# Performance work log

Measured on AMD Instinct MI355X. Metric: run time of the kernel, lower is better.

The kernel has to match this reference:

```python
import jax, jax.numpy as jnp
import numpy as np
from jax import lax

C = 128; H = 28; W = 28
VID_LENS = [32, 96, 64, 48, 80, 40, 88, 64]  # sums to 512
T_TOTAL = sum(VID_LENS)


def setup_inputs() -> dict:
    key = jax.random.key(0)
    ks = jax.random.split(key, 6)
    fan2 = C * 9
    fan1 = C * 3
    return {
        "x": jax.random.normal(ks[0], (T_TOTAL, C, H, W), dtype=jnp.float32),
        "vid_lens": jnp.array(VID_LENS, dtype=jnp.int32),
        "w_sp": jax.random.normal(ks[1], (C, C, 3, 3), dtype=jnp.float32) / np.sqrt(fan2),
        "b_sp": jax.random.normal(ks[2], (C,), dtype=jnp.float32) * 0.01,
        "w_t": jax.random.normal(ks[3], (C, C, 3), dtype=jnp.float32) / np.sqrt(fan1),
        "b_t": jax.random.normal(ks[4], (C,), dtype=jnp.float32) * 0.01,
        "alpha": jnp.full((C,), 0.25, dtype=jnp.float32),  # MultiNL ~ per-channel PReLU
    }


def _forward(x, vid_lens, w_sp, b_sp, w_t, b_t, alpha):
    projection = x
    # spatial 3x3 conv, stride 1, padding 1 (SAME), NCHW
    y = lax.conv_general_dilated(
        x, w_sp, window_strides=(1, 1), padding="SAME",
        dimension_numbers=("NCHW", "OIHW", "NCHW")) + b_sp[None, :, None, None]

    # Ragged temporal conv1d (k=3, pad=1) over concatenated time axis.
    # Zero the temporal neighbors at segment boundaries so each video is
    # convolved independently (equivalent to per-segment zero padding).
    T = y.shape[0]
    ends = jnp.cumsum(vid_lens)            # segment end indices (exclusive)
    starts = ends - vid_lens               # segment start indices
    start_mask = jnp.zeros((T,), bool).at[starts].set(True)
    end_mask = jnp.zeros((T,), bool).at[ends - 1].set(True)

    y_prev = jnp.where(start_mask[:, None, None, None], 0.0, jnp.roll(y, 1, axis=0))
    y_next = jnp.where(end_mask[:, None, None, None], 0.0, jnp.roll(y, -1, axis=0))

    # conv1d along time == per-tap channel-mixing matmul
    z = (jnp.einsum("oc,tchw->tohw", w_t[:, :, 0], y_prev)
         + jnp.einsum("oc,tchw->tohw", w_t[:, :, 1], y)
         + jnp.einsum("oc,tchw->tohw", w_t[:, :, 2], y_next)
         + b_t[None, :, None, None])

    # MultiNL modeled as per-channel PReLU
    z = jnp.where(z >= 0, z, alpha[None, :, None, None] * z)
    return z + projection


def reference(x, vid_lens, w_sp, b_sp, w_t, b_t, alpha):
    out = _forward(x, vid_lens, w_sp, b_sp, w_t, b_t, alpha)
    return (out, vid_lens)  # lengths are unchanged (k=3, pad=1)
```

## Files before the change

### kernel.cpp

```cpp
#include <hip/hip_runtime.h>

#define TT   512
#define CH   128
#define HWP  784
#define NSEG 8
#define NOUT 51380224

typedef short bf16x8  __attribute__((ext_vector_type(8)));
typedef float f32x4   __attribute__((ext_vector_type(4)));
typedef float f32x16  __attribute__((ext_vector_type(16)));
typedef int   i32x4   __attribute__((ext_vector_type(4)));
typedef unsigned short u16x4 __attribute__((ext_vector_type(4)));
typedef unsigned short u16x8 __attribute__((ext_vector_type(8)));

__device__ inline unsigned short f2bf(float f) {
    unsigned u = __builtin_bit_cast(unsigned, f);
    u += 0x7fffu + ((u >> 16) & 1u);
    return (unsigned short)(u >> 16);
}

__device__ inline void gld_lds16(const void* g, void* l) {
    __builtin_amdgcn_global_load_lds(
        (const __attribute__((address_space(1))) void*)g,
        (__attribute__((address_space(3))) void*)l, 16, 0, 0);
}

#define MFMA32(A, B, C) __builtin_amdgcn_mfma_f32_32x32x16_bf16(A, B, C, 0, 0, 0)

__global__ void repack_wsp(const float* __restrict__ w, short* __restrict__ wA) {
    int s = blockIdx.x * 256 + threadIdx.x;
    if (s >= 128 * 128 * 9) return;
    int co = s / 1152, r = s % 1152, ci = r / 9, kh = (r % 9) / 3, kw = r % 3;
    int tap = kh * 3 + kw;
    int m = co >> 5, row = co & 31;
    int ks = ci >> 4, kgrp = (ci >> 3) & 1, e = ci & 7;
    int lane = kgrp * 32 + row;
    int dst = (((tap * 8 + ks) * 4 + m) * 64 + lane) * 8 + e;
    wA[dst] = (short)f2bf(w[s]);
}

__global__ void repack_wt2(const float* __restrict__ w, short* __restrict__ wAt) {
    int s = blockIdx.x * 256 + threadIdx.x;
    if (s >= 128 * 128 * 3) return;
    int o = s / 384, r = s % 384, i = r / 3, tap = r % 3;
    int dst = tap * 16384 + (o >> 4) * 2048 + (i >> 5) * 512 +
              ((i >> 3) & 3) * 128 + (o & 15) * 8 + (i & 7);
    wAt[dst] = (short)f2bf(w[s]);
}

__global__ __launch_bounds__(256, 2) void spatial_mfma(
    const float* __restrict__ x, const short* __restrict__ wA,
    const float* __restrict__ b_sp, unsigned short* __restrict__ yT)
{
    __shared__ __align__(16) short xs[300 * 128];
    char* xsb = (char*)xs;
    const int t = blockIdx.y;
    const int r0 = blockIdx.x * 8;
    const int rows = (28 - r0 < 8) ? (28 - r0) : 8;
    const int pxcnt = rows * 28;
    const int tid = threadIdx.x;

    for (int u = tid; u < 4480; u += 256) {
        int cp = u & 63, q = u >> 6;
        int rl = q / 7, g = q % 7;
        int rr = r0 - 1 + rl;
        float4 f0 = make_float4(0.f, 0.f, 0.f, 0.f), f1 = f0;
        if (rr >= 0 && rr < 28) {
            const float* px0 = &x[((size_t)(t * CH + 2 * cp)) * HWP + rr * 28 + g * 4];
            f0 = *(const float4*)px0;
            f1 = *(const float4*)(px0 + HWP);
        }
        float a0[4] = {f0.x, f0.y, f0.z, f0.w}, a1[4] = {f1.x, f1.y, f1.z, f1.w};
        int stb = rl * 30 + g * 4 + 1;
#pragma unroll
        for (int j = 0; j < 4; ++j) {
            int st = stb + j;
            unsigned val = (unsigned)f2bf(a0[j]) | ((unsigned)f2bf(a1[j]) << 16);
            int addr = (st << 8) | (((cp >> 2) ^ (st & 15)) << 4) | ((cp & 3) << 2);
            *(unsigned*)(xsb + addr) = val;
        }
    }
    for (int v = tid; v < 1280; v += 256) {
        int cp = v & 63, k = v >> 6;
        int st = (k >> 1) * 30 + (k & 1) * 29;
        int addr = (st << 8) | (((cp >> 2) ^ (st & 15)) << 4) | ((cp & 3) << 2);
        *(unsigned*)(xsb + addr) = 0u;
    }
    __syncthreads();

    const int wid = tid >> 6, l = tid & 63;
    const int l31 = l & 31, bb5 = l >> 5;
    const int ch = wid & 1, pg = wid >> 1;
    const int ch2 = ch * 2;

    int st0[4];
#pragma unroll
    for (int ti = 0; ti < 4; ++ti) {
        int p = (pg * 4 + ti) * 32 + l31;
        int pc = (p < pxcnt) ? p : 0;
        st0[ti] = (pc / 28 + 1) * 30 + pc % 28 + 1;
    }

    f32x16 zz = {};
    f32x16 acc[2][4];
#pragma unroll
    for (int mi = 0; mi < 2; ++mi)
#pragma unroll
        for (int ti = 0; ti < 4; ++ti) acc[mi][ti] = zz;

    const bf16x8* wv = (const bf16x8*)wA;

    for (int tap = 0; tap < 9; ++tap) {
        const int off = (tap / 3 - 1) * 30 + (tap % 3) - 1;
        int rb[4], sw[4];
#pragma unroll
        for (int ti = 0; ti < 4; ++ti) {
            int stv = st0[ti] + off;
            rb[ti] = stv << 8;
            sw[ti] = stv & 15;
        }
        bf16x8 A[16];
#pragma unroll
        for (int k2 = 0; k2 < 16; ++k2)
            A[k2] = wv[((tap * 8 + (k2 >> 1)) * 4 + ch2 + (k2 & 1)) * 64 + l];

#pragma unroll
        for (int ks = 0; ks < 8; ++ks) {
            i32x4 b[4];
#pragma unroll
            for (int ti = 0; ti < 4; ++ti)
                b[ti] = *(const i32x4*)(xsb + (rb[ti] | (((2 * ks + bb5) ^ sw[ti]) << 4)));
            __builtin_amdgcn_s_setprio(1);
#pragma unroll
            for (int ti = 0; ti < 4; ++ti) {
                bf16x8 bf = __builtin_bit_cast(bf16x8, b[ti]);
                acc[0][ti] = MFMA32(A[ks * 2], bf, acc[0][ti]);
                acc[1][ti] = MFMA32(A[ks * 2 + 1], bf, acc[1][ti]);
            }
            __builtin_amdgcn_s_setprio(0);
        }
    }

    __syncthreads();
    const int wbase = wid * 17408;
#pragma unroll
    for (int ti = 0; ti < 4; ++ti) {
#pragma unroll
        for (int mi = 0; mi < 2; ++mi) {
#pragma unroll
            for (int r2 = 0; r2 < 4; ++r2) {
                int cb = (ch2 + mi) * 32 + 8 * r2 + 4 * bb5;
                float4 bs = *(const float4*)&b_sp[cb];
                float bsa[4] = {bs.x, bs.y, bs.z, bs.w};
                u16x4 k;
#pragma unroll
                for (int q = 0; q < 4; ++q)
                    k[q] = f2bf(acc[mi][ti][r2 * 4 + q] + bsa[q]);
                int co_off = (mi * 32 + 8 * r2 + 4 * bb5) * 2;
                *(u16x4*)(xsb + wbase + ti * 4352 + l31 * 136 + co_off) = k;
            }
        }
    }
#pragma unroll
    for (int ti = 0; ti < 4; ++ti) {
        int tI = pg * 4 + ti;
#pragma unroll
        for (int j = 0; j < 4; ++j) {
            int idx = j * 64 + l;
            int pxl = idx >> 3, sub = idx & 7;
            u16x8 v = *(const u16x8*)(xsb + wbase + ti * 4352 + pxl * 136 + sub * 16);
            int p = tI * 32 + pxl;
            if (p < pxcnt) {
                char* dst = (char*)yT + ((size_t)t * HWP + r0 * 28 + p) * 256 +
                            ch * 128 + sub * 16;
                *(u16x8*)dst = v;
            }
        }
    }
}

__global__ __launch_bounds__(256, 4) void temporal_mfma(
    const unsigned short* __restrict__ yT, const short* __restrict__ wAt,
    const float* __restrict__ b_t, const float* __restrict__ alpha,
    const float* __restrict__ x, const int* __restrict__ vid_lens,
    float* __restrict__ out)
{
    __shared__ __align__(16) char ldsT[29696];

    const int chunk = blockIdx.x, t = blockIdx.y;
    const int tid = threadIdx.x, wid = tid >> 6, l = tid & 63;
    const int l15 = l & 15, kgrp = l >> 4;
    const int sx = l15 & 7;

    bool isS = false, isE = false;
    {
        int cum = 0;
        for (int s = 0; s < NSEG; ++s) {
            if (t == cum) isS = true;
            cum += vid_lens[s];
            if (t == cum - 1) isE = true;
        }
    }
    const bool tapAct[3] = {!isS, true, !isE};

    auto stage = [&](int s) {
        int tap = s >> 1, kp = s & 1;
        if (!tapAct[tap]) return;
        int tp = t + tap - 1;
        const char* yb = (const char*)yT + (size_t)tp * HWP * 256;
        char* buf = ldsT + (s & 1) * 14336;
#pragma unroll
        for (int r = 0; r < 4; ++r) {
            int c = r * 256 + wid * 64 + l;
            if (r < 3 || wid < 2) {
                int px = c >> 3, sp = c & 7;
                int ssrc = sp ^ (px & 7);
                const char* g = yb + ((size_t)(chunk * 112 + px)) * 256 + kp * 128 + ssrc * 16;
                char* ldst = buf + (r * 256 + wid * 64) * 16;
                gld_lds16(g, ldst);
            }
        }
    };

    f32x4 acc[2][7];
#pragma unroll
    for (int m = 0; m < 2; ++m)
#pragma unroll
        for (int n = 0; n < 7; ++n) acc[m][n] = (f32x4){0.f, 0.f, 0.f, 0.f};

    const bf16x8* wAv = (const bf16x8*)wAt;

    stage(0);
    __syncthreads();

    for (int s = 0; s < 6; ++s) {
        if (s < 5) stage(s + 1);
        int tap = s >> 1, kp = s & 1;
        if (tapAct[tap]) {
            const char* buf = ldsT + (s & 1) * 14336;
            bf16x8 a[2][2];
#pragma unroll
            for (int m = 0; m < 2; ++m)
#pragma unroll
                for (int k1 = 0; k1 < 2; ++k1)
                    a[m][k1] = wAv[((tap * 8 + wid * 2 + m) * 4 + kp * 2 + k1) * 64 + l];
            __builtin_amdgcn_s_setprio(1);
#pragma unroll
            for (int k1 = 0; k1 < 2; ++k1) {
#pragma unroll
                for (int nf = 0; nf < 7; ++nf) {
                    int addr = (nf * 16 + l15) * 128 + ((k1 * 4 + kgrp) ^ sx) * 16;
                    i32x4 bi = *(const i32x4*)(buf + addr);
                    bf16x8 b = __builtin_bit_cast(bf16x8, bi);
                    acc[0][nf] = __builtin_amdgcn_mfma_f32_16x16x32_bf16(a[0][k1], b, acc[0][nf], 0, 0, 0);
                    acc[1][nf] = __builtin_amdgcn_mfma_f32_16x16x32_bf16(a[1][k1], b, acc[1][nf], 0, 0, 0);
                }
            }
            __builtin_amdgcn_s_setprio(0);
        }
        __syncthreads();
    }

    float* fl = (float*)ldsT;
    const int wbase = wid * 1856;
#pragma unroll
    for (int m = 0; m < 2; ++m) {
#pragma unroll
        for (int nf = 0; nf < 7; ++nf)
#pragma unroll
            for (int rr = 0; rr < 4; ++rr)
                fl[wbase + (kgrp * 4 + rr) * 116 + nf * 16 + l15] = acc[m][nf][rr];
#pragma unroll
        for (int j = 0; j < 7; ++j) {
            int idx = j * 64 + l;
            int co_r = idx / 28, q = idx % 28;
            f32x4 v4 = *(const f32x4*)&fl[wbase + co_r * 116 + q * 4];
            int co_g = wid * 32 + m * 16 + co_r;
            float bt = b_t[co_g], al = alpha[co_g];
            size_t gi = ((size_t)(t * CH + co_g)) * HWP + chunk * 112 + q * 4;
            float4 xv = *(const float4*)&x[gi];
            float xr[4] = {xv.x, xv.y, xv.z, xv.w};
            float rrv[4];
#pragma unroll
            for (int e = 0; e < 4; ++e) {
                float v = v4[e] + bt;
                v = (v >= 0.f) ? v : al * v;
                rrv[e] = v + xr[e];
            }
            *(float4*)&out[gi] = make_float4(rrv[0], rrv[1], rrv[2], rrv[3]);
        }
        __syncthreads();
    }
}

__global__ void write_lens(const int* __restrict__ vid_lens, float* __restrict__ out) {
    int i = threadIdx.x;
    if (i < NSEG) out[NOUT + i] = (float)vid_lens[i];
}

extern "C" void kernel_launch(void* const* d_in, const int* in_sizes, int n_in,
                              void* d_out, int out_size, void* d_ws, size_t ws_size,
                              hipStream_t stream) {
    const float* x        = (const float*)d_in[0];
    const int*   vid_lens = (const int*)d_in[1];
    const float* w_sp     = (const float*)d_in[2];
    const float* b_sp     = (const float*)d_in[3];
    const float* w_t      = (const float*)d_in[4];
    const float* b_t      = (const float*)d_in[5];
    const float* alpha    = (const float*)d_in[6];
    float* out = (float*)d_out;

    unsigned short* yT = (unsigned short*)d_ws;
    short* wA  = (short*)((char*)d_ws + 102760448);
    short* wAt = (short*)((char*)d_ws + 102760448 + 294912);

    repack_wsp<<<576, 256, 0, stream>>>(w_sp, wA);
    repack_wt2<<<192, 256, 0, stream>>>(w_t, wAt);
    spatial_mfma<<<dim3(4, 512), 256, 0, stream>>>(x, wA, b_sp, yT);
    temporal_mfma<<<dim3(7, 512), 256, 0, stream>>>(yT, wAt, b_t, alpha, x, vid_lens, out);
    write_lens<<<1, 64, 0, stream>>>(vid_lens, out);
}
```

Measured before the change: 336.6 us.

## Split spatial conv work across 8 waves with fewer tiles per wave

The spatial conv block grows from 256 to 512 threads. Each wave now computes 2 pixel tiles instead of 4, which halves the accumulator registers and lets more waves stay resident. Weight fragments are loaded per k-pair instead of all 16 at once, trading register pressure for more repeated global/L2 weight loads. The fp32-to-bf16 staging conversion is also changed from round-to-nearest to truncation via a byte permute, which slightly changes numerics.

```diff
diff --git a/kernel.cpp b/kernel.cpp
--- a/kernel.cpp
+++ b/kernel.cpp
@@ -48,7 +48,7 @@
     wAt[dst] = (short)f2bf(w[s]);
 }
 
-__global__ __launch_bounds__(256, 2) void spatial_mfma(
+__global__ __launch_bounds__(512, 4) void spatial_mfma(
     const float* __restrict__ x, const short* __restrict__ wA,
     const float* __restrict__ b_sp, unsigned short* __restrict__ yT)
 {
@@ -60,7 +60,7 @@
     const int pxcnt = rows * 28;
     const int tid = threadIdx.x;
 
-    for (int u = tid; u < 4480; u += 256) {
+    for (int u = tid; u < 4480; u += 512) {
         int cp = u & 63, q = u >> 6;
         int rl = q / 7, g = q % 7;
         int rr = r0 - 1 + rl;
@@ -70,17 +70,20 @@
             f0 = *(const float4*)px0;
             f1 = *(const float4*)(px0 + HWP);
         }
-        float a0[4] = {f0.x, f0.y, f0.z, f0.w}, a1[4] = {f1.x, f1.y, f1.z, f1.w};
+        unsigned u0[4] = {__builtin_bit_cast(unsigned, f0.x), __builtin_bit_cast(unsigned, f0.y),
+                          __builtin_bit_cast(unsigned, f0.z), __builtin_bit_cast(unsigned, f0.w)};
+        unsigned u1[4] = {__builtin_bit_cast(unsigned, f1.x), __builtin_bit_cast(unsigned, f1.y),
+                          __builtin_bit_cast(unsigned, f1.z), __builtin_bit_cast(unsigned, f1.w)};
         int stb = rl * 30 + g * 4 + 1;
 #pragma unroll
         for (int j = 0; j < 4; ++j) {
             int st = stb + j;
-            unsigned val = (unsigned)f2bf(a0[j]) | ((unsigned)f2bf(a1[j]) << 16);
+            unsigned val = __builtin_amdgcn_perm(u1[j], u0[j], 0x07060302u);
             int addr = (st << 8) | (((cp >> 2) ^ (st & 15)) << 4) | ((cp & 3) << 2);
             *(unsigned*)(xsb + addr) = val;
         }
     }
-    for (int v = tid; v < 1280; v += 256) {
+    for (int v = tid; v < 1280; v += 512) {
         int cp = v & 63, k = v >> 6;
         int st = (k >> 1) * 30 + (k & 1) * 29;
         int addr = (st << 8) | (((cp >> 2) ^ (st & 15)) << 4) | ((cp & 3) << 2);
@@ -92,85 +95,86 @@
     const int l31 = l & 31, bb5 = l >> 5;
     const int ch = wid & 1, pg = wid >> 1;
     const int ch2 = ch * 2;
-
-    int st0[4];
-#pragma unroll
-    for (int ti = 0; ti < 4; ++ti) {
-        int p = (pg * 4 + ti) * 32 + l31;
-        int pc = (p < pxcnt) ? p : 0;
-        st0[ti] = (pc / 28 + 1) * 30 + pc % 28 + 1;
-    }
+    const int tI0 = pg * 2, tI1 = pg * 2 + 1;
+
+    const int p0 = tI0 * 32 + l31;
+    const int p1 = tI1 * 32 + l31;
+    const bool ok0 = (p0 < pxcnt);
+    const bool ok1 = (tI1 < 7) && (p1 < pxcnt);
+    const int pc0 = ok0 ? p0 : 0;
+    const int pc1 = ok1 ? p1 : 0;
+    const int st0_0 = (pc0 / 28 + 1) * 30 + pc0 % 28 + 1;
+    const int st0_1 = (pc1 / 28 + 1) * 30 + pc1 % 28 + 1;
 
     f32x16 zz = {};
-    f32x16 acc[2][4];
-#pragma unroll
-    for (int mi = 0; mi < 2; ++mi)
-#pragma unroll
-        for (int ti = 0; ti < 4; ++ti) acc[mi][ti] = zz;
+    f32x16 acc00 = zz, acc10 = zz;
+    f32x16 acc01 = zz, acc11 = zz;
 
     const bf16x8* wv = (const bf16x8*)wA;
 
     for (int tap = 0; tap < 9; ++tap) {
         const int off = (tap / 3 - 1) * 30 + (tap % 3) - 1;
-        int rb[4], sw[4];
-#pragma unroll
-        for (int ti = 0; ti < 4; ++ti) {
-            int stv = st0[ti] + off;
-            rb[ti] = stv << 8;
-            sw[ti] = stv & 15;
-        }
-        bf16x8 A[16];
-#pragma unroll
-        for (int k2 = 0; k2 < 16; ++k2)
-            A[k2] = wv[((tap * 8 + (k2 >> 1)) * 4 + ch2 + (k2 & 1)) * 64 + l];
-
-#pragma unroll
-        for (int ks = 0; ks < 8; ++ks) {
-            i32x4 b[4];
-#pragma unroll
-            for (int ti = 0; ti < 4; ++ti)
-                b[ti] = *(const i32x4*)(xsb + (rb[ti] | (((2 * ks + bb5) ^ sw[ti]) << 4)));
+        const int stv0 = st0_0 + off, stv1 = st0_1 + off;
+        const int rb0 = stv0 << 8, sw0 = stv0 & 15;
+        const int rb1 = stv1 << 8, sw1 = stv1 & 15;
+#pragma unroll
+        for (int kp = 0; kp < 4; ++kp) {
+            const int ks0 = kp * 2, ks1 = kp * 2 + 1;
+            bf16x8 A00 = wv[((tap * 8 + ks0) * 4 + ch2 + 0) * 64 + l];
+            bf16x8 A01 = wv[((tap * 8 + ks0) * 4 + ch2 + 1) * 64 + l];
+            bf16x8 A10 = wv[((tap * 8 + ks1) * 4 + ch2 + 0) * 64 + l];
+            bf16x8 A11 = wv[((tap * 8 + ks1) * 4 + ch2 + 1) * 64 + l];
+            i32x4 b00 = *(const i32x4*)(xsb + (rb0 | (((ks0 * 2 + bb5) ^ sw0) << 4)));
+            i32x4 b01 = *(const i32x4*)(xsb + (rb0 | (((ks1 * 2 + bb5) ^ sw0) << 4)));
+            i32x4 b10 = *(const i32x4*)(xsb + (rb1 | (((ks0 * 2 + bb5) ^ sw1) << 4)));
+            i32x4 b11 = *(const i32x4*)(xsb + (rb1 | (((ks1 * 2 + bb5) ^ sw1) << 4)));
+            bf16x8 f00 = __builtin_bit_cast(bf16x8, b00);
+            bf16x8 f01 = __builtin_bit_cast(bf16x8, b01);
+            bf16x8 f10 = __builtin_bit_cast(bf16x8, b10);
+            bf16x8 f11 = __builtin_bit_cast(bf16x8, b11);
             __builtin_amdgcn_s_setprio(1);
-#pragma unroll
-            for (int ti = 0; ti < 4; ++ti) {
-                bf16x8 bf = __builtin_bit_cast(bf16x8, b[ti]);
-                acc[0][ti] = MFMA32(A[ks * 2], bf, acc[0][ti]);
-                acc[1][ti] = MFMA32(A[ks * 2 + 1], bf, acc[1][ti]);
-            }
+            acc00 = MFMA32(A00, f00, acc00);
+            acc10 = MFMA32(A01, f00, acc10);
+            acc01 = MFMA32(A00, f10, acc01);
+            acc11 = MFMA32(A01, f10, acc11);
+            acc00 = MFMA32(A10, f01, acc00);
+            acc10 = MFMA32(A11, f01, acc10);
+            acc01 = MFMA32(A10, f11, acc01);
+            acc11 = MFMA32(A11, f11, acc11);
             __builtin_amdgcn_s_setprio(0);
         }
     }
 
     __syncthreads();
-    const int wbase = wid * 17408;
-#pragma unroll
-    for (int ti = 0; ti < 4; ++ti) {
-#pragma unroll
-        for (int mi = 0; mi < 2; ++mi) {
-#pragma unroll
-            for (int r2 = 0; r2 < 4; ++r2) {
-                int cb = (ch2 + mi) * 32 + 8 * r2 + 4 * bb5;
-                float4 bs = *(const float4*)&b_sp[cb];
-                float bsa[4] = {bs.x, bs.y, bs.z, bs.w};
-                u16x4 k;
-#pragma unroll
-                for (int q = 0; q < 4; ++q)
-                    k[q] = f2bf(acc[mi][ti][r2 * 4 + q] + bsa[q]);
-                int co_off = (mi * 32 + 8 * r2 + 4 * bb5) * 2;
-                *(u16x4*)(xsb + wbase + ti * 4352 + l31 * 136 + co_off) = k;
-            }
-        }
-    }
-#pragma unroll
-    for (int ti = 0; ti < 4; ++ti) {
-        int tI = pg * 4 + ti;
+    const int wbase = wid * 8704;
+#pragma unroll
+    for (int mi = 0; mi < 2; ++mi) {
+#pragma unroll
+        for (int r2 = 0; r2 < 4; ++r2) {
+            int cb = (ch2 + mi) * 32 + 8 * r2 + 4 * bb5;
+            float4 bs = *(const float4*)&b_sp[cb];
+            float bsa[4] = {bs.x, bs.y, bs.z, bs.w};
+            u16x4 k0, k1;
+#pragma unroll
+            for (int q = 0; q < 4; ++q) {
+                k0[q] = f2bf((mi ? acc10[r2 * 4 + q] : acc00[r2 * 4 + q]) + bsa[q]);
+                k1[q] = f2bf((mi ? acc11[r2 * 4 + q] : acc01[r2 * 4 + q]) + bsa[q]);
+            }
+            int co_off = (mi * 32 + 8 * r2 + 4 * bb5) * 2;
+            *(u16x4*)(xsb + wbase + l31 * 136 + co_off) = k0;
+            *(u16x4*)(xsb + wbase + 4352 + l31 * 136 + co_off) = k1;
+        }
+    }
+#pragma unroll
+    for (int tt2 = 0; tt2 < 2; ++tt2) {
+        int tI = tt2 ? tI1 : tI0;
 #pragma unroll
         for (int j = 0; j < 4; ++j) {
             int idx = j * 64 + l;
             int pxl = idx >> 3, sub = idx & 7;
-            u16x8 v = *(const u16x8*)(xsb + wbase + ti * 4352 + pxl * 136 + sub * 16);
+            u16x8 v = *(const u16x8*)(xsb + wbase + tt2 * 4352 + pxl * 136 + sub * 16);
             int p = tI * 32 + pxl;
-            if (p < pxcnt) {
+            if (tI < 7 && p < pxcnt) {
                 char* dst = (char*)yT + ((size_t)t * HWP + r0 * 28 + p) * 256 +
                             ch * 128 + sub * 16;
                 *(u16x8*)dst = v;
@@ -316,7 +320,7 @@
 
     repack_wsp<<<576, 256, 0, stream>>>(w_sp, wA);
     repack_wt2<<<192, 256, 0, stream>>>(w_t, wAt);
-    spatial_mfma<<<dim3(4, 512), 256, 0, stream>>>(x, wA, b_sp, yT);
+    spatial_mfma<<<dim3(4, 512), 512, 0, stream>>>(x, wA, b_sp, yT);
     temporal_mfma<<<dim3(7, 512), 256, 0, stream>>>(yT, wAt, b_t, alpha, x, vid_lens, out);
     write_lens<<<1, 64, 0, stream>>>(vid_lens, out);
 }
```

Result: no change. 337.4 us (+0.2%).
